# Performance work log

Hardware: AMD Instinct MI355X
Metric: run time of the kernel (lower is better)

The kernel has to match this reference:

```python
import jax, jax.numpy as jnp
import numpy as np
from jax import lax

B, T, I, H = 32, 512, 256, 512


def setup_inputs() -> dict:
    key = jax.random.key(0)
    ks = jax.random.split(key, 6)
    s_ih = 1.0 / np.sqrt(I)
    s_hh = 1.0 / np.sqrt(H)
    return {
        "x": jax.random.normal(ks[0], (B, T, I), dtype=jnp.float32),
        "W_ih_f": jax.random.normal(ks[1], (4 * H, I), dtype=jnp.float32) * s_ih,
        "W_hh_f": jax.random.normal(ks[2], (4 * H, H), dtype=jnp.float32) * s_hh,
        "b_f": jnp.zeros((4 * H,), dtype=jnp.float32),
        "W_ih_b": jax.random.normal(ks[3], (4 * H, I), dtype=jnp.float32) * s_ih,
        "W_hh_b": jax.random.normal(ks[4], (4 * H, H), dtype=jnp.float32) * s_hh,
        "b_b": jnp.zeros((4 * H,), dtype=jnp.float32),
    }


def _lstm(x, W_ih, W_hh, b):
    # x: [B, T, I] -> hidden sequence [B, T, H]
    Bx, Tx, _ = x.shape
    Hh = W_hh.shape[1]
    # precompute input projections for all timesteps: [T, B, 4H]
    x_proj = jnp.einsum('bti,gi->tbg', x, W_ih) + b

    def step(carry, xp):
        h, c = carry
        gates = xp + h @ W_hh.T  # [B, 4H]
        i, f, g, o = jnp.split(gates, 4, axis=-1)
        i = jax.nn.sigmoid(i)
        f = jax.nn.sigmoid(f)
        g = jnp.tanh(g)
        o = jax.nn.sigmoid(o)
        c = f * c + i * g
        h = o * jnp.tanh(c)
        return (h, c), h

    h0 = jnp.zeros((Bx, Hh), dtype=x.dtype)
    c0 = jnp.zeros((Bx, Hh), dtype=x.dtype)
    _, hs = lax.scan(step, (h0, c0), x_proj)  # hs: [T, B, H]
    return hs.transpose(1, 0, 2)


def reference(x, W_ih_f, W_hh_f, b_f, W_ih_b, W_hh_b, b_b):
    out_fwd = _lstm(x, W_ih_f, W_hh_f, b_f)                      # [B, T, H]
    x_rev = jnp.flip(x, axis=1)
    out_bwd = jnp.flip(_lstm(x_rev, W_ih_b, W_hh_b, b_b), axis=1)  # [B, T, H]
    return jnp.concatenate((out_fwd, out_bwd), axis=2)           # [B, T, 2H]
```

## Files before the change

kernel.cpp:

```cpp
#include <hip/hip_runtime.h>

#define B_    32
#define T_    512
#define I_    256
#define H_    512
#define PB    16
#define NBLK  32
#define NT    256
#define NSLOT 4
#define HPITCH 34

typedef __attribute__((ext_vector_type(8))) short  short8;
typedef __attribute__((ext_vector_type(4))) float  float4v;

__device__ __forceinline__ unsigned short f2bf(float f) {
    union { float f; unsigned u; } v; v.f = f;
    unsigned r = v.u + 0x7FFFu + ((v.u >> 16) & 1u);
    return (unsigned short)(r >> 16);
}

__device__ __forceinline__ short8 cvt8(const float* p) {
    float4 u = *reinterpret_cast<const float4*>(p);
    float4 v = *reinterpret_cast<const float4*>(p + 4);
    short8 r;
    r[0] = (short)f2bf(u.x); r[1] = (short)f2bf(u.y);
    r[2] = (short)f2bf(u.z); r[3] = (short)f2bf(u.w);
    r[4] = (short)f2bf(v.x); r[5] = (short)f2bf(v.y);
    r[6] = (short)f2bf(v.z); r[7] = (short)f2bf(v.w);
    return r;
}

__device__ __forceinline__ unsigned long long pack4bf(float a, float b, float c, float d) {
    return (unsigned long long)f2bf(a)
         | ((unsigned long long)f2bf(b) << 16)
         | ((unsigned long long)f2bf(c) << 32)
         | ((unsigned long long)f2bf(d) << 48);
}

__device__ __forceinline__ float sigm(float v)  { return 1.0f / (1.0f + __expf(-v)); }
__device__ __forceinline__ float tanhf_(float v){ return 2.0f / (1.0f + __expf(-2.0f * v)) - 1.0f; }

__global__ __launch_bounds__(256) void build_xfrag(const float* __restrict__ x,
                                                   unsigned short* __restrict__ xf) {
    const int t = blockIdx.x, tid = threadIdx.x;
#pragma unroll
    for (int rep = 0; rep < 4; ++rep) {
        const int eidx  = rep * 256 + tid;
        const int chunk = eidx >> 6, lf = eidx & 63;
        const int kstep = chunk >> 1, nh = chunk & 1;
        const int kq = lf >> 4, nm = lf & 15;
        const int b  = nh * 16 + nm;
        const int i0 = kstep * 32 + kq * 8;
        short8 v = cvt8(x + ((size_t)b * T_ + t) * I_ + i0);
        *reinterpret_cast<short8*>(xf + ((size_t)t * 16 + chunk) * 512 + lf * 8) = v;
    }
}

__global__ __launch_bounds__(NT, 1) void bilstm_mfma(
    const float* __restrict__ Wih_f, const float* __restrict__ Whh_f, const float* __restrict__ bias_f,
    const float* __restrict__ Wih_b, const float* __restrict__ Whh_b, const float* __restrict__ bias_b,
    float* __restrict__ out, float* __restrict__ ws) {

    __shared__ __align__(16) char  sAX[16 * 1024];
    __shared__ __align__(16) char  sAH[32 * 1024];
    __shared__ __align__(16) float sHT[B_ * HPITCH];

    const int tid  = threadIdx.x;
    const int lane = tid & 63;
    const int w    = tid >> 6;
    const int d    = blockIdx.x & 1;
    const int pb   = blockIdx.x >> 1;

    const unsigned short* xfrag = (const unsigned short*)ws;
    unsigned long long* hfrag = (unsigned long long*)((char*)ws + (size_t)T_ * 16 * 1024);
    const char* hfrag_b = (const char*)hfrag;
    unsigned* bar = (unsigned*)((char*)hfrag + (size_t)2 * NSLOT * 32 * 1024);

    const float* Wih = d ? Wih_b : Wih_f;
    const float* Whh = d ? Whh_b : Whh_f;
    const float* bia = d ? bias_b : bias_f;

    const int mA  = lane & 15;
    const int kqA = lane >> 4;
    const int gA  = mA & 3;
    const int gr0 = gA * H_ + 32 * pb + 8 * w + (mA >> 2);
    const int gr1 = gr0 + 4;

    short8 wx0[8], wx1[8], wh0[16], wh1[16];
#pragma unroll
    for (int kst = 0; kst < 8; ++kst) {
        wx0[kst] = cvt8(Wih + (size_t)gr0 * I_ + kst * 32 + kqA * 8);
        wx1[kst] = cvt8(Wih + (size_t)gr1 * I_ + kst * 32 + kqA * 8);
    }
#pragma unroll
    for (int kst = 0; kst < 16; ++kst) {
        wh0[kst] = cvt8(Whh + (size_t)gr0 * H_ + kst * 32 + kqA * 8);
        wh1[kst] = cvt8(Whh + (size_t)gr1 * H_ + kst * 32 + kqA * 8);
    }

    const int hid0 = 32 * pb + 8 * w + kqA;
    float4v bq0, bq1;
#pragma unroll
    for (int g = 0; g < 4; ++g) {
        bq0[g] = bia[g * H_ + hid0];
        bq1[g] = bia[g * H_ + hid0 + 4];
    }

    const int pub_b  = tid & 31;
    const int pub_r8 = tid >> 5;
    const unsigned pub_chunkL = pb * 2 + (pub_b >> 4);
    const unsigned pub_lf     = pub_r8 * 16 + (pub_b & 15);

    float c00 = 0.f, c01 = 0.f, c10 = 0.f, c11 = 0.f;
    __syncthreads();

    for (int t = 0; t < T_; ++t) {
        const int tx    = d ? (T_ - 1 - t) : t;
        const int slot  = t & (NSLOT - 1);
        const int pslot = (t - 1) & (NSLOT - 1);

        {
            const char* src = (const char*)xfrag + ((size_t)tx * 16 + w * 4) * 1024 + lane * 16;
            uint4 xbuf[4];
#pragma unroll
            for (int c = 0; c < 4; ++c) xbuf[c] = *reinterpret_cast<const uint4*>(src + c * 1024);
#pragma unroll
            for (int c = 0; c < 4; ++c)
                *reinterpret_cast<uint4*>(sAX + (w * 4 + c) * 1024 + lane * 16) = xbuf[c];
        }

        if (t > 0 && tid == 0) {
            while (__hip_atomic_load(&bar[d * T_ + (t - 1)], __ATOMIC_RELAXED,
                                     __HIP_MEMORY_SCOPE_AGENT) < PB)
                __builtin_amdgcn_s_sleep(1);
        }
        __syncthreads();

        unsigned long long hbuf[16];
        if (t > 0) {
            const char* src = hfrag_b + ((size_t)(d * NSLOT + pslot) * 32 + w * 8) * 1024 + lane * 16;
#pragma unroll
            for (int c = 0; c < 8; ++c) {
                hbuf[2 * c + 0] = __hip_atomic_load((const unsigned long long*)(src + c * 1024),
                                                    __ATOMIC_RELAXED, __HIP_MEMORY_SCOPE_AGENT);
                hbuf[2 * c + 1] = __hip_atomic_load((const unsigned long long*)(src + c * 1024 + 8),
                                                    __ATOMIC_RELAXED, __HIP_MEMORY_SCOPE_AGENT);
            }
        }

        float4v a00 = bq0, a01 = bq0, a10 = bq1, a11 = bq1;
#pragma unroll
        for (int kst = 0; kst < 8; ++kst) {
            short8 f0 = *reinterpret_cast<const short8*>(sAX + (kst * 2 + 0) * 1024 + lane * 16);
            short8 f1 = *reinterpret_cast<const short8*>(sAX + (kst * 2 + 1) * 1024 + lane * 16);
            a00 = __builtin_amdgcn_mfma_f32_16x16x32_bf16(wx0[kst], f0, a00, 0, 0, 0);
            a01 = __builtin_amdgcn_mfma_f32_16x16x32_bf16(wx0[kst], f1, a01, 0, 0, 0);
            a10 = __builtin_amdgcn_mfma_f32_16x16x32_bf16(wx1[kst], f0, a10, 0, 0, 0);
            a11 = __builtin_amdgcn_mfma_f32_16x16x32_bf16(wx1[kst], f1, a11, 0, 0, 0);
        }

        if (t > 0) {
#pragma unroll
            for (int c = 0; c < 8; ++c) {
                char* dst = sAH + (w * 8 + c) * 1024 + lane * 16;
                *reinterpret_cast<unsigned long long*>(dst)     = hbuf[2 * c + 0];
                *reinterpret_cast<unsigned long long*>(dst + 8) = hbuf[2 * c + 1];
            }
        }
        __syncthreads();

        if (t > 0) {
#pragma unroll
            for (int kst = 0; kst < 16; ++kst) {
                short8 f0 = *reinterpret_cast<const short8*>(sAH + (kst * 2 + 0) * 1024 + lane * 16);
                short8 f1 = *reinterpret_cast<const short8*>(sAH + (kst * 2 + 1) * 1024 + lane * 16);
                a00 = __builtin_amdgcn_mfma_f32_16x16x32_bf16(wh0[kst], f0, a00, 0, 0, 0);
                a01 = __builtin_amdgcn_mfma_f32_16x16x32_bf16(wh0[kst], f1, a01, 0, 0, 0);
                a10 = __builtin_amdgcn_mfma_f32_16x16x32_bf16(wh1[kst], f0, a10, 0, 0, 0);
                a11 = __builtin_amdgcn_mfma_f32_16x16x32_bf16(wh1[kst], f1, a11, 0, 0, 0);
            }
        }

        float h00, h01, h10, h11;
        {
            float iv, fv, gv, ov, c;
            iv = sigm(a00[0]); fv = sigm(a00[1]); gv = tanhf_(a00[2]); ov = sigm(a00[3]);
            c = fv * c00 + iv * gv; c00 = c; h00 = ov * tanhf_(c);
            iv = sigm(a01[0]); fv = sigm(a01[1]); gv = tanhf_(a01[2]); ov = sigm(a01[3]);
            c = fv * c01 + iv * gv; c01 = c; h01 = ov * tanhf_(c);
            iv = sigm(a10[0]); fv = sigm(a10[1]); gv = tanhf_(a10[2]); ov = sigm(a10[3]);
            c = fv * c10 + iv * gv; c10 = c; h10 = ov * tanhf_(c);
            iv = sigm(a11[0]); fv = sigm(a11[1]); gv = tanhf_(a11[2]); ov = sigm(a11[3]);
            c = fv * c11 + iv * gv; c11 = c; h11 = ov * tanhf_(c);
        }

        {
            const int hl = 8 * w + kqA;
            const int bn = mA;
            sHT[(bn)      * HPITCH + hl]     = h00;
            sHT[(bn + 16) * HPITCH + hl]     = h01;
            sHT[(bn)      * HPITCH + hl + 4] = h10;
            sHT[(bn + 16) * HPITCH + hl + 4] = h11;
        }
        __syncthreads();

        float2 f01, f23, f45, f67;
        if (tid < 128) {
            const float* rp = sHT + pub_b * HPITCH + 8 * pub_r8;
            f01 = *reinterpret_cast<const float2*>(rp + 0);
            f23 = *reinterpret_cast<const float2*>(rp + 2);
            f45 = *reinterpret_cast<const float2*>(rp + 4);
            f67 = *reinterpret_cast<const float2*>(rp + 6);
            const unsigned long long lo = pack4bf(f01.x, f01.y, f23.x, f23.y);
            const unsigned long long hi = pack4bf(f45.x, f45.y, f67.x, f67.y);
            char* dst = (char*)hfrag + ((size_t)((d * NSLOT + slot) * 32 + pub_chunkL)) * 1024
                      + pub_lf * 16;
            __hip_atomic_store((unsigned long long*)dst,       lo, __ATOMIC_RELAXED, __HIP_MEMORY_SCOPE_AGENT);
            __hip_atomic_store((unsigned long long*)(dst + 8), hi, __ATOMIC_RELAXED, __HIP_MEMORY_SCOPE_AGENT);
        }
        __syncthreads();

        if (tid == 0)
            __hip_atomic_fetch_add(&bar[d * T_ + t], 1u, __ATOMIC_RELAXED,
                                   __HIP_MEMORY_SCOPE_AGENT);

        if (tid < 128) {
            float* op = out + ((size_t)pub_b * T_ + tx) * (2 * H_) + (size_t)d * H_
                      + 32 * pb + 8 * pub_r8;
            *reinterpret_cast<float4*>(op + 0) = make_float4(f01.x, f01.y, f23.x, f23.y);
            *reinterpret_cast<float4*>(op + 4) = make_float4(f45.x, f45.y, f67.x, f67.y);
        }
    }
}

extern "C" void kernel_launch(void* const* d_in, const int* in_sizes, int n_in,
                              void* d_out, int out_size, void* d_ws, size_t ws_size,
                              hipStream_t stream) {
    const float* x     = (const float*)d_in[0];
    const float* Wih_f = (const float*)d_in[1];
    const float* Whh_f = (const float*)d_in[2];
    const float* b_f   = (const float*)d_in[3];
    const float* Wih_b = (const float*)d_in[4];
    const float* Whh_b = (const float*)d_in[5];
    const float* b_b   = (const float*)d_in[6];
    float* out = (float*)d_out;

    const size_t xf_bytes = (size_t)T_ * 16 * 1024;
    const size_t hf_bytes = (size_t)2 * NSLOT * 32 * 1024;
    const size_t bar_bytes = (size_t)2 * T_ * sizeof(unsigned);

    hipMemsetAsync((char*)d_ws + xf_bytes + hf_bytes, 0, bar_bytes, stream);

    hipLaunchKernelGGL(build_xfrag, dim3(T_), dim3(256), 0, stream,
                       x, (unsigned short*)d_ws);

    hipLaunchKernelGGL(bilstm_mfma, dim3(NBLK), dim3(NT), 0, stream,
                       Wih_f, Whh_f, b_f, Wih_b, Whh_b, b_b, out, (float*)d_ws);
}
```

Baseline: 2.423 ms.

## Precompute next-step input projection after publishing h, prefetch x two steps ahead

Moves the input-projection MFMAs (W_ih·x_t) out of the latency-critical span between the barrier wait and the recurrent matmul. They now run after h for step t is published, while other blocks are still finishing. The x fragments are prefetched into registers two steps ahead so the global load latency is hidden. This costs an extra __syncthreads per step and extra registers for the prefetch buffer and the accumulators carried across iterations.

```diff
diff --git a/kernel.cpp b/kernel.cpp
--- a/kernel.cpp
+++ b/kernel.cpp
@@ -71,7 +71,7 @@
     const int d    = blockIdx.x & 1;
     const int pb   = blockIdx.x >> 1;
 
-    const unsigned short* xfrag = (const unsigned short*)ws;
+    const char* xfrag_b = (const char*)ws;
     unsigned long long* hfrag = (unsigned long long*)((char*)ws + (size_t)T_ * 16 * 1024);
     const char* hfrag_b = (const char*)hfrag;
     unsigned* bar = (unsigned*)((char*)hfrag + (size_t)2 * NSLOT * 32 * 1024);
@@ -111,23 +111,43 @@
     const unsigned pub_chunkL = pb * 2 + (pub_b >> 4);
     const unsigned pub_lf     = pub_r8 * 16 + (pub_b & 15);
 
+    {
+        const int tx0 = d ? (T_ - 1) : 0;
+        const char* src = xfrag_b + ((size_t)tx0 * 16 + w * 4) * 1024 + lane * 16;
+#pragma unroll
+        for (int c = 0; c < 4; ++c) {
+            uint4 v = *reinterpret_cast<const uint4*>(src + c * 1024);
+            *reinterpret_cast<uint4*>(sAX + (w * 4 + c) * 1024 + lane * 16) = v;
+        }
+    }
+    __syncthreads();
+
+    float4v xa00 = bq0, xa01 = bq0, xa10 = bq1, xa11 = bq1;
+#pragma unroll
+    for (int kst = 0; kst < 8; ++kst) {
+        short8 f0 = *reinterpret_cast<const short8*>(sAX + (kst * 2 + 0) * 1024 + lane * 16);
+        short8 f1 = *reinterpret_cast<const short8*>(sAX + (kst * 2 + 1) * 1024 + lane * 16);
+        xa00 = __builtin_amdgcn_mfma_f32_16x16x32_bf16(wx0[kst], f0, xa00, 0, 0, 0);
+        xa01 = __builtin_amdgcn_mfma_f32_16x16x32_bf16(wx0[kst], f1, xa01, 0, 0, 0);
+        xa10 = __builtin_amdgcn_mfma_f32_16x16x32_bf16(wx1[kst], f0, xa10, 0, 0, 0);
+        xa11 = __builtin_amdgcn_mfma_f32_16x16x32_bf16(wx1[kst], f1, xa11, 0, 0, 0);
+    }
+
+    uint4 xpre[4];
+    {
+        const int tx1 = d ? (T_ - 2) : 1;
+        const char* src = xfrag_b + ((size_t)tx1 * 16 + w * 4) * 1024 + lane * 16;
+#pragma unroll
+        for (int c = 0; c < 4; ++c)
+            xpre[c] = *reinterpret_cast<const uint4*>(src + c * 1024);
+    }
+
     float c00 = 0.f, c01 = 0.f, c10 = 0.f, c11 = 0.f;
-    __syncthreads();
 
     for (int t = 0; t < T_; ++t) {
         const int tx    = d ? (T_ - 1 - t) : t;
         const int slot  = t & (NSLOT - 1);
         const int pslot = (t - 1) & (NSLOT - 1);
-
-        {
-            const char* src = (const char*)xfrag + ((size_t)tx * 16 + w * 4) * 1024 + lane * 16;
-            uint4 xbuf[4];
-#pragma unroll
-            for (int c = 0; c < 4; ++c) xbuf[c] = *reinterpret_cast<const uint4*>(src + c * 1024);
-#pragma unroll
-            for (int c = 0; c < 4; ++c)
-                *reinterpret_cast<uint4*>(sAX + (w * 4 + c) * 1024 + lane * 16) = xbuf[c];
-        }
 
         if (t > 0 && tid == 0) {
             while (__hip_atomic_load(&bar[d * T_ + (t - 1)], __ATOMIC_RELAXED,
@@ -146,20 +166,6 @@
                 hbuf[2 * c + 1] = __hip_atomic_load((const unsigned long long*)(src + c * 1024 + 8),
                                                     __ATOMIC_RELAXED, __HIP_MEMORY_SCOPE_AGENT);
             }
-        }
-
-        float4v a00 = bq0, a01 = bq0, a10 = bq1, a11 = bq1;
-#pragma unroll
-        for (int kst = 0; kst < 8; ++kst) {
-            short8 f0 = *reinterpret_cast<const short8*>(sAX + (kst * 2 + 0) * 1024 + lane * 16);
-            short8 f1 = *reinterpret_cast<const short8*>(sAX + (kst * 2 + 1) * 1024 + lane * 16);
-            a00 = __builtin_amdgcn_mfma_f32_16x16x32_bf16(wx0[kst], f0, a00, 0, 0, 0);
-            a01 = __builtin_amdgcn_mfma_f32_16x16x32_bf16(wx0[kst], f1, a01, 0, 0, 0);
-            a10 = __builtin_amdgcn_mfma_f32_16x16x32_bf16(wx1[kst], f0, a10, 0, 0, 0);
-            a11 = __builtin_amdgcn_mfma_f32_16x16x32_bf16(wx1[kst], f1, a11, 0, 0, 0);
-        }
-
-        if (t > 0) {
 #pragma unroll
             for (int c = 0; c < 8; ++c) {
                 char* dst = sAH + (w * 8 + c) * 1024 + lane * 16;
@@ -168,6 +174,8 @@
             }
         }
         __syncthreads();
+
+        float4v a00 = xa00, a01 = xa01, a10 = xa10, a11 = xa11;
 
         if (t > 0) {
 #pragma unroll
@@ -230,6 +238,32 @@
             *reinterpret_cast<float4*>(op + 0) = make_float4(f01.x, f01.y, f23.x, f23.y);
             *reinterpret_cast<float4*>(op + 4) = make_float4(f45.x, f45.y, f67.x, f67.y);
         }
+
+        if (t + 1 < T_) {
+#pragma unroll
+            for (int c = 0; c < 4; ++c)
+                *reinterpret_cast<uint4*>(sAX + (w * 4 + c) * 1024 + lane * 16) = xpre[c];
+
+            if (t + 2 < T_) {
+                const int txn2 = d ? (T_ - 3 - t) : (t + 2);
+                const char* src = xfrag_b + ((size_t)txn2 * 16 + w * 4) * 1024 + lane * 16;
+#pragma unroll
+                for (int c = 0; c < 4; ++c)
+                    xpre[c] = *reinterpret_cast<const uint4*>(src + c * 1024);
+            }
+            __syncthreads();
+
+            xa00 = bq0; xa01 = bq0; xa10 = bq1; xa11 = bq1;
+#pragma unroll
+            for (int kst = 0; kst < 8; ++kst) {
+                short8 f0 = *reinterpret_cast<const short8*>(sAX + (kst * 2 + 0) * 1024 + lane * 16);
+                short8 f1 = *reinterpret_cast<const short8*>(sAX + (kst * 2 + 1) * 1024 + lane * 16);
+                xa00 = __builtin_amdgcn_mfma_f32_16x16x32_bf16(wx0[kst], f0, xa00, 0, 0, 0);
+                xa01 = __builtin_amdgcn_mfma_f32_16x16x32_bf16(wx0[kst], f1, xa01, 0, 0, 0);
+                xa10 = __builtin_amdgcn_mfma_f32_16x16x32_bf16(wx1[kst], f0, xa10, 0, 0, 0);
+                xa11 = __builtin_amdgcn_mfma_f32_16x16x32_bf16(wx1[kst], f1, xa11, 0, 0, 0);
+            }
+        }
     }
 }
 
@@ -245,8 +279,8 @@
     const float* b_b   = (const float*)d_in[6];
     float* out = (float*)d_out;
 
-    const size_t xf_bytes = (size_t)T_ * 16 * 1024;
-    const size_t hf_bytes = (size_t)2 * NSLOT * 32 * 1024;
+    const size_t xf_bytes  = (size_t)T_ * 16 * 1024;
+    const size_t hf_bytes  = (size_t)2 * NSLOT * 32 * 1024;
     const size_t bar_bytes = (size_t)2 * T_ * sizeof(unsigned);
 
     hipMemsetAsync((char*)d_ws + xf_bytes + hf_bytes, 0, bar_bytes, stream);
```

After: 2.468 ms. Within noise of the previous version (+1.9%).
